# Optimization experiments

Measured on AMD Instinct MI355X. Metric: run time of the kernel, lower is better.

## Reference

```python
import jax, jax.numpy as jnp
import numpy as np

HEADS = 16
DIM_HEAD = 64
SCALE = DIM_HEAD ** -0.5


def setup_inputs() -> dict:
    key = jax.random.key(0)
    ks = jax.random.split(key, 6)
    d = 1024
    x = jax.random.normal(ks[0], (4, 2048, d), dtype=jnp.float32)
    s = d ** -0.5
    Wq = jax.random.normal(ks[1], (d, d), dtype=jnp.float32) * s
    Wk = jax.random.normal(ks[2], (d, d), dtype=jnp.float32) * s
    Wv = jax.random.normal(ks[3], (d, d), dtype=jnp.float32) * s
    Wo = jax.random.normal(ks[4], (d, d), dtype=jnp.float32) * s
    bo = jnp.zeros((d,), dtype=jnp.float32)
    return {"x": x, "Wq": Wq, "Wk": Wk, "Wv": Wv, "Wo": Wo, "bo": bo}


def reference(x, Wq, Wk, Wv, Wo, bo):
    b, n, _ = x.shape
    h, dh = HEADS, DIM_HEAD
    # projections (bias-free), split heads: b n (h d) -> b h n d
    def split(t):
        return t.reshape(b, n, h, dh).transpose(0, 2, 1, 3)
    q = split(x @ Wq.T)
    k = split(x @ Wk.T)
    v = split(x @ Wv.T)
    # fp32 scores (inputs already fp32; explicit cast mirrors ATTN_PRECISION='fp32')
    sim = jnp.einsum('bhid,bhjd->bhij', q.astype(jnp.float32), k.astype(jnp.float32)) * SCALE
    attn = jax.nn.softmax(sim, axis=-1)
    out = jnp.einsum('bhij,bhjd->bhid', attn, v)
    out = out.transpose(0, 2, 1, 3).reshape(b, n, h * dh)
    return out @ Wo.T + bo
```

## Files before the change

### kernel.cpp

```cpp
#include <hip/hip_runtime.h>

typedef float f32x4 __attribute__((ext_vector_type(4)));
typedef short s16x8 __attribute__((ext_vector_type(8)));
typedef __bf16 bf16x8 __attribute__((ext_vector_type(8)));
typedef unsigned int u32;
typedef unsigned short u16;

struct __align__(8) us4 { u16 s[4]; };

#define DEVINL static __device__ __forceinline__

DEVINL f32x4 mfma_bf16(s16x8 a, s16x8 b, f32x4 c) {
  return __builtin_amdgcn_mfma_f32_16x16x32_bf16(
      __builtin_bit_cast(bf16x8, a), __builtin_bit_cast(bf16x8, b), c, 0, 0, 0);
}

DEVINL u16 f2bf(float f) {
  __bf16 h = (__bf16)f;
  return __builtin_bit_cast(u16, h);
}

DEVINL float exp2_fast(float x) {
  float r;
  asm("v_exp_f32 %0, %1" : "=v"(r) : "v"(x));
  return r;
}

#define GLD16(gp, lp)                                                         \
  __builtin_amdgcn_global_load_lds(                                           \
      (const __attribute__((address_space(1))) void*)(gp),                    \
      (__attribute__((address_space(3))) void*)(lp), 16, 0, 0)

#define PIPE_BAR()                                                            \
  do {                                                                        \
    asm volatile("s_waitcnt vmcnt(0)" ::: "memory");                          \
    __builtin_amdgcn_sched_barrier(0);                                        \
    __builtin_amdgcn_s_barrier();                                             \
    __builtin_amdgcn_sched_barrier(0);                                        \
  } while (0)

__global__ __launch_bounds__(256) void convert_k(
    const float* __restrict__ x, const float* __restrict__ wq,
    const float* __restrict__ wk, const float* __restrict__ wv,
    const float* __restrict__ wo, u16* __restrict__ xb,
    u16* __restrict__ wqkv, u16* __restrict__ wob) {
  long i = (long)blockIdx.x * 256 + threadIdx.x;
  const float4* s;
  u16* d;
  if (i < 2097152) {
    s = (const float4*)x + i; d = xb + i * 4;
  } else if (i < 2359296) {
    long j = i - 2097152; s = (const float4*)wq + j; d = wqkv + j * 4;
  } else if (i < 2621440) {
    long j = i - 2359296; s = (const float4*)wk + j; d = wqkv + 1048576 + j * 4;
  } else if (i < 2883584) {
    long j = i - 2621440; s = (const float4*)wv + j; d = wqkv + 2097152 + j * 4;
  } else {
    long j = i - 2883584; s = (const float4*)wo + j; d = wob + j * 4;
  }
  float4 v = *s;
  us4 w;
  w.s[0] = f2bf(v.x); w.s[1] = f2bf(v.y); w.s[2] = f2bf(v.z); w.s[3] = f2bf(v.w);
  *(us4*)d = w;
}

template <int MODE>
__global__ __launch_bounds__(256, 2) void gemm_bt(
    const u16* __restrict__ A, const u16* __restrict__ B,
    u16* __restrict__ oq, u16* __restrict__ ok, u16* __restrict__ ovt,
    float* __restrict__ oc, const float* __restrict__ bias) {
  __shared__ __align__(16) u16 lA[128 * 64];
  __shared__ __align__(16) u16 lB[128 * 64];
  const int t = threadIdx.x;
  const int wave = t >> 6, lane = t & 63, g = lane >> 4, c = lane & 15;
  const int bm = blockIdx.y, bn = blockIdx.x;
  const int wr = wave >> 1, wc = wave & 1;
  f32x4 acc[4][4] = {};
  const long arow0 = (long)bm * 128;
  const long brow0 = (long)bn * 128;

  for (int kk = 0; kk < 1024; kk += 64) {
    __syncthreads();
#pragma unroll
    for (int i = 0; i < 4; ++i) {
      int s = i * 256 + t;
      int row = s >> 3, ch = s & 7;
      int gc = (ch ^ (row & 7)) * 8;
      GLD16(A + (arow0 + row) * 1024 + kk + gc, lA + (i * 256 + wave * 64) * 8);
      GLD16(B + (brow0 + row) * 1024 + kk + gc, lB + (i * 256 + wave * 64) * 8);
    }
    __syncthreads();
#pragma unroll
    for (int k2 = 0; k2 < 2; ++k2) {
      s16x8 af[4], bfr[4];
#pragma unroll
      for (int m = 0; m < 4; ++m) {
        int r = wr * 64 + m * 16 + c;
        af[m] = *(const s16x8*)&lA[r * 64 + (((k2 * 4 + g) ^ (r & 7)) * 8)];
      }
#pragma unroll
      for (int n = 0; n < 4; ++n) {
        int r = wc * 64 + n * 16 + c;
        bfr[n] = *(const s16x8*)&lB[r * 64 + (((k2 * 4 + g) ^ (r & 7)) * 8)];
      }
#pragma unroll
      for (int m = 0; m < 4; ++m)
#pragma unroll
        for (int n = 0; n < 4; ++n)
          acc[m][n] = mfma_bf16(af[m], bfr[n], acc[m][n]);
    }
  }

  if (MODE == 0) {
    const float SQ = 0.18033688011112042f;
#pragma unroll
    for (int n = 0; n < 4; ++n) {
      int colb = bn * 128 + wc * 64 + n * 16;
      int tsel = colb >> 10;
      int f = colb & 1023;
      int h = f >> 6, d0 = f & 63;
#pragma unroll
      for (int m = 0; m < 4; ++m) {
        int row = bm * 128 + wr * 64 + m * 16 + g * 4;
        int b = row >> 11, nn = row & 2047;
        if (tsel == 0) {
          long base = ((long)(b * 16 + h) * 2048 + nn) * 64 + d0 + c;
#pragma unroll
          for (int j = 0; j < 4; ++j)
            oq[base + (long)j * 64] = f2bf(acc[m][n][j] * SQ);
        } else if (tsel == 1) {
          long base = ((long)(b * 16 + h) * 2048 + nn) * 64 + d0 + c;
#pragma unroll
          for (int j = 0; j < 4; ++j)
            ok[base + (long)j * 64] = f2bf(acc[m][n][j]);
        } else {
          us4 w;
#pragma unroll
          for (int j = 0; j < 4; ++j) w.s[j] = f2bf(acc[m][n][j]);
          *(us4*)&ovt[((long)(b * 16 + h) * 64 + d0 + c) * 2048 + nn] = w;
        }
      }
    }
  } else {
#pragma unroll
    for (int n = 0; n < 4; ++n) {
      int col = bn * 128 + wc * 64 + n * 16 + c;
      float bv = bias[col];
#pragma unroll
      for (int m = 0; m < 4; ++m) {
        int row = bm * 128 + wr * 64 + m * 16 + g * 4;
#pragma unroll
        for (int j = 0; j < 4; ++j)
          oc[(long)(row + j) * 1024 + col] = acc[m][n][j] + bv;
      }
    }
  }
}

__global__ __launch_bounds__(256, 2) void flash_attn(
    const u16* __restrict__ q, const u16* __restrict__ k,
    const u16* __restrict__ vt, u16* __restrict__ ao) {
  __shared__ __align__(16) u16 lKV[2 * 8192];
  __shared__ __align__(16) u16 lP[4 * 2176];
  const int t = threadIdx.x;
  const int wave = t >> 6, lane = t & 63, g = lane >> 4, c = lane & 15;
  const int wg = blockIdx.x;
  const int bh = wg & 63, qt = wg >> 6;

  const u16* kb = k + (long)bh * (2048 * 64);
  const u16* vb = vt + (long)bh * (64 * 2048);

  const int srow = t >> 3, sch = t & 7;
  const int sgc = (sch ^ (srow & 7)) * 8;
  const u16* kp = kb + srow * 64 + sgc;
  const u16* vp = vb + srow * 2048 + sgc;

  auto stage = [&](u16* lb) {
    GLD16(kp, lb + wave * 512);
    GLD16(kp + 2048, lb + 2048 + wave * 512);
    GLD16(vp, lb + 4096 + wave * 512);
    GLD16(vp + 65536, lb + 6144 + wave * 512);
    kp += 4096;
    vp += 64;
  };

  const u16* qp = q + ((long)bh * 2048 + qt * 128 + wave * 32) * 64;
  s16x8 bq[2][2];
#pragma unroll
  for (int qn = 0; qn < 2; ++qn)
#pragma unroll
    for (int k2 = 0; k2 < 2; ++k2)
      bq[qn][k2] = *(const s16x8*)(qp + (qn * 16 + c) * 64 + k2 * 32 + g * 8);

  int kread[2];
  kread[0] = c * 64 + ((g ^ (c & 7)) * 8);
  kread[1] = c * 64 + (((4 + g) ^ (c & 7)) * 8);
  const int wp = wave * 2176 + c * 68 + g * 4;
  const int rp = wave * 2176 + c * 68 + g * 8;

  float m_[2] = {-3e38f, -3e38f}, ls[2] = {0.f, 0.f};
  f32x4 ov[4][2] = {};

  auto do_tile = [&](const u16* lb) {
    f32x4 st[4][2] = {};
#pragma unroll
    for (int k2 = 0; k2 < 2; ++k2) {
      s16x8 ak[4];
#pragma unroll
      for (int mk = 0; mk < 4; ++mk)
        ak[mk] = *(const s16x8*)&lb[kread[k2] + mk * 1024];
#pragma unroll
      for (int mk = 0; mk < 4; ++mk)
#pragma unroll
        for (int qn = 0; qn < 2; ++qn)
          st[mk][qn] = mfma_bf16(ak[mk], bq[qn][k2], st[mk][qn]);
    }
#pragma unroll
    for (int qn = 0; qn < 2; ++qn) {
      f32x4 m4 = st[0][qn];
#pragma unroll
      for (int mk = 1; mk < 4; ++mk) {
        m4[0] = fmaxf(m4[0], st[mk][qn][0]);
        m4[1] = fmaxf(m4[1], st[mk][qn][1]);
        m4[2] = fmaxf(m4[2], st[mk][qn][2]);
        m4[3] = fmaxf(m4[3], st[mk][qn][3]);
      }
      float tm = fmaxf(fmaxf(m4[0], m4[1]), fmaxf(m4[2], m4[3]));
      tm = fmaxf(tm, __shfl_xor(tm, 16));
      tm = fmaxf(tm, __shfl_xor(tm, 32));
      if (__any(tm > m_[qn] + 8.0f)) {
        float mn = fmaxf(m_[qn], tm);
        float al = exp2_fast(m_[qn] - mn);
        m_[qn] = mn;
        ls[qn] *= al;
#pragma unroll
        for (int mo = 0; mo < 4; ++mo) ov[mo][qn] *= al;
      }
      float m0 = m_[qn], ps = 0.f;
#pragma unroll
      for (int mk = 0; mk < 4; ++mk) {
        float p0 = exp2_fast(st[mk][qn][0] - m0);
        float p1 = exp2_fast(st[mk][qn][1] - m0);
        float p2 = exp2_fast(st[mk][qn][2] - m0);
        float p3 = exp2_fast(st[mk][qn][3] - m0);
        ps += (p0 + p1) + (p2 + p3);
        us4 w;
        w.s[0] = f2bf(p0); w.s[1] = f2bf(p1);
        w.s[2] = f2bf(p2); w.s[3] = f2bf(p3);
        *(us4*)&lP[wp + qn * 1088 + mk * 16] = w;
      }
      ps += __shfl_xor(ps, 16);
      ps += __shfl_xor(ps, 32);
      ls[qn] += ps;
    }
#pragma unroll
    for (int k2 = 0; k2 < 2; ++k2) {
      s16x8 bp[2];
#pragma unroll
      for (int qn = 0; qn < 2; ++qn)
        bp[qn] = *(const s16x8*)&lP[rp + qn * 1088 + k2 * 32];
#pragma unroll
      for (int mo = 0; mo < 4; ++mo) {
        s16x8 av = *(const s16x8*)&lb[4096 + kread[k2] + mo * 1024];
#pragma unroll
        for (int qn = 0; qn < 2; ++qn)
          ov[mo][qn] = mfma_bf16(av, bp[qn], ov[mo][qn]);
      }
    }
  };

  stage(lKV);
  PIPE_BAR();
#pragma unroll 1
  for (int it = 0; it < 16; ++it) {
    stage(lKV + 8192);
    do_tile(lKV);
    PIPE_BAR();
    if (it < 15) stage(lKV);
    do_tile(lKV + 8192);
    PIPE_BAR();
  }

  int b = bh >> 4, h = bh & 15;
  u16* ob = ao + ((long)b * 2048 + qt * 128 + wave * 32) * 1024 + h * 64;
#pragma unroll
  for (int qn = 0; qn < 2; ++qn) {
    float inv = 1.0f / ls[qn];
#pragma unroll
    for (int mo = 0; mo < 4; ++mo) {
      us4 w;
#pragma unroll
      for (int j = 0; j < 4; ++j) w.s[j] = f2bf(ov[mo][qn][j] * inv);
      *(us4*)&ob[(long)(qn * 16 + c) * 1024 + mo * 16 + g * 4] = w;
    }
  }
}

extern "C" void kernel_launch(void* const* d_in, const int* in_sizes, int n_in,
                              void* d_out, int out_size, void* d_ws, size_t ws_size,
                              hipStream_t stream) {
  const float* x = (const float*)d_in[0];
  const float* wq = (const float*)d_in[1];
  const float* wk = (const float*)d_in[2];
  const float* wv = (const float*)d_in[3];
  const float* wo = (const float*)d_in[4];
  const float* bo = (const float*)d_in[5];
  char* ws = (char*)d_ws;
  u16* xb   = (u16*)(ws);
  u16* wqkv = (u16*)(ws + (16l << 20));
  u16* wob  = (u16*)(ws + (22l << 20));
  u16* qb   = (u16*)(ws + (24l << 20));
  u16* kbuf = (u16*)(ws + (40l << 20));
  u16* vtb  = (u16*)(ws + (56l << 20));
  u16* aob  = (u16*)(ws + (72l << 20));
  float* out = (float*)d_out;

  convert_k<<<12288, 256, 0, stream>>>(x, wq, wk, wv, wo, xb, wqkv, wob);
  gemm_bt<0><<<dim3(24, 64), 256, 0, stream>>>(xb, wqkv, qb, kbuf, vtb,
                                               nullptr, nullptr);
  flash_attn<<<1024, 256, 0, stream>>>(qb, kbuf, vtb, aob);
  gemm_bt<1><<<dim3(8, 64), 256, 0, stream>>>(aob, wob, nullptr, nullptr,
                                              nullptr, out, bo);
}
```

Baseline: 198.7 us.

## Switch flash attention to 32x32 MFMA with register-resident P via permlane swap

Rewrites the attention inner loop to use 32x32x16 bf16 MFMA tiles instead of 16x16x32. The probability matrix is repacked in registers with v_permlane32_swap, so it no longer round-trips through LDS, and the lP shared buffer is removed. Each lane now holds one query row, which simplifies the row max and sum reductions. It also raises the occupancy hint to 4 blocks per SM and adds s_setprio around the MFMA sections. Register pressure may rise, and the register layout of P is tricky to get right.

After: 185.1 us. 1.07x faster.

```diff
diff --git a/kernel.cpp b/kernel.cpp
--- a/kernel.cpp
+++ b/kernel.cpp
@@ -1,9 +1,11 @@
 #include <hip/hip_runtime.h>
 
 typedef float f32x4 __attribute__((ext_vector_type(4)));
+typedef float f32x16 __attribute__((ext_vector_type(16)));
 typedef short s16x8 __attribute__((ext_vector_type(8)));
 typedef __bf16 bf16x8 __attribute__((ext_vector_type(8)));
 typedef unsigned int u32;
+typedef unsigned int u32x4 __attribute__((ext_vector_type(4)));
 typedef unsigned short u16;
 
 struct __align__(8) us4 { u16 s[4]; };
@@ -15,9 +17,22 @@
       __builtin_bit_cast(bf16x8, a), __builtin_bit_cast(bf16x8, b), c, 0, 0, 0);
 }
 
+DEVINL f32x16 mfma32_bf16(s16x8 a, s16x8 b, f32x16 c) {
+  return __builtin_amdgcn_mfma_f32_32x32x16_bf16(
+      __builtin_bit_cast(bf16x8, a), __builtin_bit_cast(bf16x8, b), c, 0, 0, 0);
+}
+
 DEVINL u16 f2bf(float f) {
   __bf16 h = (__bf16)f;
   return __builtin_bit_cast(u16, h);
+}
+
+DEVINL u32 pk2(float a, float b) {
+  return (u32)f2bf(a) | ((u32)f2bf(b) << 16);
+}
+
+DEVINL void pl32swap(u32& a, u32& b) {
+  asm volatile("v_permlane32_swap_b32 %0, %1" : "+v"(a), "+v"(b));
 }
 
 DEVINL float exp2_fast(float x) {
@@ -157,13 +172,13 @@
   }
 }
 
-__global__ __launch_bounds__(256, 2) void flash_attn(
+__global__ __launch_bounds__(256, 4) void flash_attn(
     const u16* __restrict__ q, const u16* __restrict__ k,
     const u16* __restrict__ vt, u16* __restrict__ ao) {
   __shared__ __align__(16) u16 lKV[2 * 8192];
-  __shared__ __align__(16) u16 lP[4 * 2176];
   const int t = threadIdx.x;
-  const int wave = t >> 6, lane = t & 63, g = lane >> 4, c = lane & 15;
+  const int wave = t >> 6, lane = t & 63;
+  const int lc = lane & 31, hi = lane >> 5, x7 = lc & 7;
   const int wg = blockIdx.x;
   const int bh = wg & 63, qt = wg >> 6;
 
@@ -184,89 +199,78 @@
     vp += 64;
   };
 
-  const u16* qp = q + ((long)bh * 2048 + qt * 128 + wave * 32) * 64;
-  s16x8 bq[2][2];
-#pragma unroll
-  for (int qn = 0; qn < 2; ++qn)
-#pragma unroll
-    for (int k2 = 0; k2 < 2; ++k2)
-      bq[qn][k2] = *(const s16x8*)(qp + (qn * 16 + c) * 64 + k2 * 32 + g * 8);
-
-  int kread[2];
-  kread[0] = c * 64 + ((g ^ (c & 7)) * 8);
-  kread[1] = c * 64 + (((4 + g) ^ (c & 7)) * 8);
-  const int wp = wave * 2176 + c * 68 + g * 4;
-  const int rp = wave * 2176 + c * 68 + g * 8;
-
-  float m_[2] = {-3e38f, -3e38f}, ls[2] = {0.f, 0.f};
-  f32x4 ov[4][2] = {};
+  const u16* qp =
+      q + ((long)bh * 2048 + qt * 128 + wave * 32 + lc) * 64 + hi * 8;
+  s16x8 bq[4];
+#pragma unroll
+  for (int kd = 0; kd < 4; ++kd) bq[kd] = *(const s16x8*)(qp + kd * 16);
+
+  float m_ = -3e38f, ls = 0.f;
+  f32x16 o[2] = {};
 
   auto do_tile = [&](const u16* lb) {
-    f32x4 st[4][2] = {};
-#pragma unroll
-    for (int k2 = 0; k2 < 2; ++k2) {
-      s16x8 ak[4];
-#pragma unroll
-      for (int mk = 0; mk < 4; ++mk)
-        ak[mk] = *(const s16x8*)&lb[kread[k2] + mk * 1024];
-#pragma unroll
-      for (int mk = 0; mk < 4; ++mk)
-#pragma unroll
-        for (int qn = 0; qn < 2; ++qn)
-          st[mk][qn] = mfma_bf16(ak[mk], bq[qn][k2], st[mk][qn]);
-    }
-#pragma unroll
-    for (int qn = 0; qn < 2; ++qn) {
-      f32x4 m4 = st[0][qn];
-#pragma unroll
-      for (int mk = 1; mk < 4; ++mk) {
-        m4[0] = fmaxf(m4[0], st[mk][qn][0]);
-        m4[1] = fmaxf(m4[1], st[mk][qn][1]);
-        m4[2] = fmaxf(m4[2], st[mk][qn][2]);
-        m4[3] = fmaxf(m4[3], st[mk][qn][3]);
-      }
-      float tm = fmaxf(fmaxf(m4[0], m4[1]), fmaxf(m4[2], m4[3]));
-      tm = fmaxf(tm, __shfl_xor(tm, 16));
-      tm = fmaxf(tm, __shfl_xor(tm, 32));
-      if (__any(tm > m_[qn] + 8.0f)) {
-        float mn = fmaxf(m_[qn], tm);
-        float al = exp2_fast(m_[qn] - mn);
-        m_[qn] = mn;
-        ls[qn] *= al;
-#pragma unroll
-        for (int mo = 0; mo < 4; ++mo) ov[mo][qn] *= al;
-      }
-      float m0 = m_[qn], ps = 0.f;
-#pragma unroll
-      for (int mk = 0; mk < 4; ++mk) {
-        float p0 = exp2_fast(st[mk][qn][0] - m0);
-        float p1 = exp2_fast(st[mk][qn][1] - m0);
-        float p2 = exp2_fast(st[mk][qn][2] - m0);
-        float p3 = exp2_fast(st[mk][qn][3] - m0);
-        ps += (p0 + p1) + (p2 + p3);
-        us4 w;
-        w.s[0] = f2bf(p0); w.s[1] = f2bf(p1);
-        w.s[2] = f2bf(p2); w.s[3] = f2bf(p3);
-        *(us4*)&lP[wp + qn * 1088 + mk * 16] = w;
-      }
-      ps += __shfl_xor(ps, 16);
-      ps += __shfl_xor(ps, 32);
-      ls[qn] += ps;
-    }
-#pragma unroll
-    for (int k2 = 0; k2 < 2; ++k2) {
-      s16x8 bp[2];
-#pragma unroll
-      for (int qn = 0; qn < 2; ++qn)
-        bp[qn] = *(const s16x8*)&lP[rp + qn * 1088 + k2 * 32];
-#pragma unroll
-      for (int mo = 0; mo < 4; ++mo) {
-        s16x8 av = *(const s16x8*)&lb[4096 + kread[k2] + mo * 1024];
-#pragma unroll
-        for (int qn = 0; qn < 2; ++qn)
-          ov[mo][qn] = mfma_bf16(av, bp[qn], ov[mo][qn]);
-      }
-    }
+    f32x16 st[2] = {};
+    __builtin_amdgcn_s_setprio(1);
+#pragma unroll
+    for (int ks = 0; ks < 2; ++ks)
+#pragma unroll
+      for (int kd = 0; kd < 4; ++kd) {
+        s16x8 ak =
+            *(const s16x8*)&lb[(ks * 32 + lc) * 64 + (((kd * 2 + hi) ^ x7) * 8)];
+        st[ks] = mfma32_bf16(ak, bq[kd], st[ks]);
+      }
+    __builtin_amdgcn_s_setprio(0);
+
+    float tm = st[0][0];
+#pragma unroll
+    for (int i = 1; i < 16; ++i) tm = fmaxf(tm, st[0][i]);
+#pragma unroll
+    for (int i = 0; i < 16; ++i) tm = fmaxf(tm, st[1][i]);
+    tm = fmaxf(tm, __shfl_xor(tm, 32));
+    if (__any(tm > m_ + 8.0f)) {
+      float mn = fmaxf(m_, tm);
+      float al = exp2_fast(m_ - mn);
+      m_ = mn;
+      ls *= al;
+#pragma unroll
+      for (int i = 0; i < 16; ++i) o[0][i] *= al;
+#pragma unroll
+      for (int i = 0; i < 16; ++i) o[1][i] *= al;
+    }
+    float ps = 0.f;
+#pragma unroll
+    for (int ks = 0; ks < 2; ++ks)
+#pragma unroll
+      for (int i = 0; i < 16; ++i) {
+        float p = exp2_fast(st[ks][i] - m_);
+        st[ks][i] = p;
+        ps += p;
+      }
+    ps += __shfl_xor(ps, 32);
+    ls += ps;
+
+    __builtin_amdgcn_s_setprio(1);
+#pragma unroll
+    for (int ks2 = 0; ks2 < 4; ++ks2) {
+      const f32x16& P = st[ks2 >> 1];
+      const int b0 = (ks2 & 1) * 8;
+      u32 A0 = pk2(P[b0 + 0], P[b0 + 1]);
+      u32 B0 = pk2(P[b0 + 2], P[b0 + 3]);
+      u32 A1 = pk2(P[b0 + 4], P[b0 + 5]);
+      u32 B1 = pk2(P[b0 + 6], P[b0 + 7]);
+      pl32swap(A0, A1);
+      pl32swap(B0, B1);
+      u32x4 pw;
+      pw[0] = A0; pw[1] = B0; pw[2] = A1; pw[3] = B1;
+      s16x8 bp = __builtin_bit_cast(s16x8, pw);
+#pragma unroll
+      for (int do2 = 0; do2 < 2; ++do2) {
+        s16x8 av = *(const s16x8*)&lb[4096 + (do2 * 32 + lc) * 64 +
+                                      (((ks2 * 2 + hi) ^ x7) * 8)];
+        o[do2] = mfma32_bf16(av, bp, o[do2]);
+      }
+    }
+    __builtin_amdgcn_s_setprio(0);
   };
 
   stage(lKV);
@@ -282,18 +286,18 @@
   }
 
   int b = bh >> 4, h = bh & 15;
-  u16* ob = ao + ((long)b * 2048 + qt * 128 + wave * 32) * 1024 + h * 64;
-#pragma unroll
-  for (int qn = 0; qn < 2; ++qn) {
-    float inv = 1.0f / ls[qn];
-#pragma unroll
-    for (int mo = 0; mo < 4; ++mo) {
+  u16* ob = ao + ((long)b * 2048 + qt * 128 + wave * 32 + lc) * 1024 + h * 64 +
+            hi * 4;
+  float inv = 1.0f / ls;
+#pragma unroll
+  for (int do2 = 0; do2 < 2; ++do2)
+#pragma unroll
+    for (int tq = 0; tq < 4; ++tq) {
       us4 w;
 #pragma unroll
-      for (int j = 0; j < 4; ++j) w.s[j] = f2bf(ov[mo][qn][j] * inv);
-      *(us4*)&ob[(long)(qn * 16 + c) * 1024 + mo * 16 + g * 4] = w;
-    }
-  }
+      for (int j = 0; j < 4; ++j) w.s[j] = f2bf(o[do2][tq * 4 + j] * inv);
+      *(us4*)&ob[do2 * 32 + tq * 8] = w;
+    }
 }
 
 extern "C" void kernel_launch(void* const* d_in, const int* in_sizes, int n_in,
```
